# Kernel tuning notes

Measured on AMD Instinct MI355X. Metric: run time of the kernel, lower is better.

The kernel has to match this reference:

```python
import itertools
import jax, jax.numpy as jnp
import numpy as np

N_OBJECTS = 32
GRAPHLET_SIZE = 3
N_FILTERS = 16
REL_DIM = 16
BATCH = 32
N_GROUP_QUERIES = 512
BETA = 1.0

# static combinatorial groups: all C(32,3) = 4960 index triples
GROUP_IDX = jnp.asarray(
    np.array(list(itertools.combinations(range(N_OBJECTS), GRAPHLET_SIZE)), dtype=np.int32)
)  # (G, g)


def setup_inputs() -> dict:
    key = jax.random.key(0)
    k1, k2, k3 = jax.random.split(key, 3)
    inputs = jax.random.normal(k1, (BATCH, N_OBJECTS, N_OBJECTS, REL_DIM), dtype=jnp.float32)
    group_logits = jax.random.normal(k2, (N_GROUP_QUERIES, N_OBJECTS), dtype=jnp.float32)
    filters = jax.random.normal(k3, (N_FILTERS, GRAPHLET_SIZE, GRAPHLET_SIZE, REL_DIM), dtype=jnp.float32)
    return {"inputs": inputs, "group_logits": group_logits, "filters": filters}


def reference(inputs, group_logits, filters):
    idx = GROUP_IDX  # (G, g)
    # gather sub-relation tensors for every group in one fused advanced-index:
    # (B, G, g, g, D)
    sub_rel = inputs[:, idx[:, :, None], idx[:, None, :], :]
    # relational inner product with all filters: (B, G, F)
    rel_conv = jnp.einsum('bgijd,fijd->bgf', sub_rel, filters)
    # soft group weights
    sp = jax.nn.softplus(group_logits)            # (Gi, N)
    group_obj_w = sp[:, idx]                      # (Gi, G, g) -- gather along object axis
    group_w = jnp.prod(group_obj_w, axis=-1)      # (Gi, G)
    norm_w = jax.nn.softmax(BETA * group_w, axis=-1)  # (Gi, G)
    # contract over combinatorial groups: (B, Gi, F)
    out = jnp.einsum('bnr,gn->bgr', rel_conv, norm_w)
    return out
```

## Files before the change

### kernel.cpp

```cpp
#include <hip/hip_runtime.h>
#include <hip/hip_bf16.h>

#define N_OBJ   32
#define G_TOTAL 4960
#define GPAD    5120
#define N_FILT  16
#define REL_D   16
#define BATCH   32
#define NQ      512
#define ZSPLIT  16
#define KCH     320
#define NIT     10

typedef __attribute__((ext_vector_type(8))) short bf16x8;
typedef __attribute__((ext_vector_type(4))) float f32x4;

static __device__ inline unsigned short f2bf(float x) {
    union { float f; unsigned int u; } v; v.f = x;
    unsigned int r = v.u + 0x7fffu + ((v.u >> 16) & 1u);
    return (unsigned short)(r >> 16);
}
static __device__ inline float bfbits2f(unsigned int bits) {
    union { unsigned int u; float f; } v; v.u = bits; return v.f;
}
static __device__ inline void gload_lds16(const void* g, void* l) {
    __builtin_amdgcn_global_load_lds(
        (const __attribute__((address_space(1))) unsigned int*)g,
        (__attribute__((address_space(3))) unsigned int*)(unsigned int)(uintptr_t)l,
        16, 0, 0);
}
static __device__ inline void unrank3(int g, int& a, int& b, int& c) {
    int rem = g;
    for (a = 0; a < 30; a++) { int cnt = ((31 - a) * (30 - a)) >> 1; if (rem < cnt) break; rem -= cnt; }
    for (b = a + 1; b < 31; b++) { if (rem < 31 - b) break; rem -= 31 - b; }
    c = b + 1 + rem;
}

__global__ __launch_bounds__(256) void k_front(const float* __restrict__ logits,
                                               const float* __restrict__ inputs,
                                               const float* __restrict__ filters,
                                               unsigned short* __restrict__ normw,
                                               unsigned short* __restrict__ D) {
    __shared__ __align__(16) char smem[11648];
    int t = threadIdx.x;
    int role = blockIdx.x;

    if (role < NQ) {
        float* sp  = (float*)smem;
        float* red = (float*)(smem + 128);
        unsigned short* wrow = (unsigned short*)(smem + 144);
        int q = role;
        if (t < N_OBJ) {
            float x = logits[q * N_OBJ + t];
            sp[t] = (x > 15.f) ? x : log1pf(expf(x));
        }
        if (t < GPAD - G_TOTAL) wrow[G_TOTAL + t] = 0;
        __syncthreads();

        int g0 = t * 20;
        int aa, bb, cc;
        unrank3(g0, aa, bb, cc);

        float w[20];
        float lmax = -1e30f;
#pragma unroll
        for (int k = 0; k < 20; k++) {
            float v = -1e30f;
            if (g0 + k < G_TOTAL) v = sp[aa] * sp[bb] * sp[cc];
            w[k] = v;
            lmax = fmaxf(lmax, v);
            cc++;
            if (cc >= 32) { bb++; cc = bb + 1; if (cc >= 32) { aa++; bb = aa + 1; cc = bb + 1; } }
        }
#pragma unroll
        for (int off = 32; off; off >>= 1) lmax = fmaxf(lmax, __shfl_down(lmax, off, 64));
        if ((t & 63) == 0) red[t >> 6] = lmax;
        __syncthreads();
        float wmax = fmaxf(fmaxf(red[0], red[1]), fmaxf(red[2], red[3]));

        float lsum = 0.f;
#pragma unroll
        for (int k = 0; k < 20; k++) {
            float e = (g0 + k < G_TOTAL) ? expf(w[k] - wmax) : 0.f;
            w[k] = e;
            lsum += e;
        }
#pragma unroll
        for (int off = 32; off; off >>= 1) lsum += __shfl_down(lsum, off, 64);
        __syncthreads();
        if ((t & 63) == 0) red[t >> 6] = lsum;
        __syncthreads();
        float inv = 1.f / (red[0] + red[1] + red[2] + red[3]);

#pragma unroll
        for (int k = 0; k < 20; k++)
            if (g0 + k < G_TOTAL) wrow[g0 + k] = f2bf(w[k] * inv);
        __syncthreads();
        uint4* dstrow = (uint4*)(normw + (size_t)q * GPAD);
        const uint4* srow = (const uint4*)wrow;
        for (int i = t; i < 640; i += 256) dstrow[i] = srow[i];
    } else {
        float* flt = (float*)smem;
        int bid = role - NQ;
        int p = bid >> 7;
        int xb = bid & 127;
        for (int i = t; i < 576; i += 256) {
            int i4 = i * 4;
            int f = i4 / 144;
            int r = i4 - f * 144;
            *(float4*)&flt[f * 180 + (r >> 4) * 20 + (r & 15)] = *(const float4*)(filters + i4);
        }
        __syncthreads();

        int row = xb * 256 + t;
        int b = row >> 10, xy = row & 1023;
        const float4* src = (const float4*)(inputs + (size_t)row * 16);
        float4 s0 = src[0], s1 = src[1], s2 = src[2], s3 = src[3];

        unsigned short outv[16];
        const float* fb = &flt[p * 20];
#pragma unroll
        for (int f = 0; f < 16; f++) {
            float4 f0 = *(const float4*)(fb + f * 180);
            float4 f1 = *(const float4*)(fb + f * 180 + 4);
            float4 f2 = *(const float4*)(fb + f * 180 + 8);
            float4 f3 = *(const float4*)(fb + f * 180 + 12);
            float d = s0.x * f0.x + s0.y * f0.y + s0.z * f0.z + s0.w * f0.w;
            d += s1.x * f1.x + s1.y * f1.y + s1.z * f1.z + s1.w * f1.w;
            d += s2.x * f2.x + s2.y * f2.y + s2.z * f2.z + s2.w * f2.w;
            d += s3.x * f3.x + s3.y * f3.y + s3.z * f3.z + s3.w * f3.w;
            outv[f] = f2bf(d);
        }
        uint4* dst = (uint4*)(D + ((size_t)(xy * 9 + p)) * 512 + b * 16);
        dst[0] = ((uint4*)outv)[0];
        dst[1] = ((uint4*)outv)[1];
    }
}

__global__ __launch_bounds__(256) void k_mid(const unsigned short* __restrict__ D,
                                             unsigned short* __restrict__ relT) {
    __shared__ int tri[8];
    int t = threadIdx.x;
    int g0 = blockIdx.x * 8;
    if (t < 8) {
        int a, b, c;
        unrank3(g0 + t, a, b, c);
        tri[t] = a | (b << 8) | (c << 16);
    }
    __syncthreads();

    float s0[8], s1[8];
#pragma unroll
    for (int g = 0; g < 8; g++) {
        int pk = tri[g];
        int xs[3] = { pk & 255, (pk >> 8) & 255, (pk >> 16) & 255 };
        float x0 = 0.f, x1 = 0.f;
#pragma unroll
        for (int i = 0; i < 3; i++)
#pragma unroll
            for (int j = 0; j < 3; j++) {
                int xy = xs[i] * 32 + xs[j];
                unsigned int v = *(const unsigned int*)(D + (size_t)(xy * 9 + i * 3 + j) * 512 + t * 2);
                x0 += bfbits2f(v << 16);
                x1 += bfbits2f(v & 0xffff0000u);
            }
        s0[g] = x0; s1[g] = x1;
    }
    unsigned int pack0[4], pack1[4];
#pragma unroll
    for (int k = 0; k < 4; k++) {
        pack0[k] = f2bf(s0[2 * k]) | ((unsigned int)f2bf(s0[2 * k + 1]) << 16);
        pack1[k] = f2bf(s1[2 * k]) | ((unsigned int)f2bf(s1[2 * k + 1]) << 16);
    }
    *(uint4*)(relT + (size_t)(2 * t) * GPAD + g0)     = *(uint4*)pack0;
    *(uint4*)(relT + (size_t)(2 * t + 1) * GPAD + g0) = *(uint4*)pack1;
}

__global__ __launch_bounds__(256) void k_gemm(const unsigned short* __restrict__ A,
                                              const unsigned short* __restrict__ Bm,
                                              float* __restrict__ part) {
    __shared__ __align__(16) unsigned short As[2][64 * 32];
    __shared__ __align__(16) unsigned short Bs[2][64 * 32];
    int tid = threadIdx.x;
    int q0 = blockIdx.x * 64, n0 = blockIdx.y * 64, z = blockIdx.z;
    int k0 = z * KCH;
    int wave = tid >> 6, lane = tid & 63;
    int wm = wave & 1, wn = wave >> 1;
    int row16 = lane & 15, quad = lane >> 4;

    int srow = tid >> 2;
    int schunk = (tid & 3) ^ ((srow >> 1) & 3);
    const unsigned short* ga = A + (size_t)(q0 + srow) * GPAD + k0 + schunk * 8;
    const unsigned short* gb = Bm + (size_t)(n0 + srow) * GPAD + k0 + schunk * 8;
    char* lA = (char*)&As[0][0] + tid * 16;
    char* lB = (char*)&Bs[0][0] + tid * 16;

    f32x4 acc[2][2] = {};
    int fchunk = (quad ^ ((row16 >> 1) & 3)) * 8;

    gload_lds16(ga, lA);
    gload_lds16(gb, lB);
    for (int it = 0; it < NIT; ++it) {
        __syncthreads();
        if (it + 1 < NIT) {
            int nb = (it + 1) & 1;
            gload_lds16(ga + (it + 1) * 32, lA + nb * 64 * 32 * 2);
            gload_lds16(gb + (it + 1) * 32, lB + nb * 64 * 32 * 2);
        }
        int buf = it & 1;
        bf16x8 afr[2], bfr[2];
#pragma unroll
        for (int mi = 0; mi < 2; mi++)
            afr[mi] = *(const bf16x8*)&As[buf][(wm * 32 + mi * 16 + row16) * 32 + fchunk];
#pragma unroll
        for (int ni = 0; ni < 2; ni++)
            bfr[ni] = *(const bf16x8*)&Bs[buf][(wn * 32 + ni * 16 + row16) * 32 + fchunk];
#pragma unroll
        for (int mi = 0; mi < 2; mi++)
#pragma unroll
            for (int ni = 0; ni < 2; ni++)
                acc[mi][ni] = __builtin_amdgcn_mfma_f32_16x16x32_bf16(
                    afr[mi], bfr[ni], acc[mi][ni], 0, 0, 0);
    }

    float* pz = part + (size_t)z * (NQ * 512);
#pragma unroll
    for (int mi = 0; mi < 2; mi++)
#pragma unroll
        for (int ni = 0; ni < 2; ni++)
#pragma unroll
            for (int r = 0; r < 4; r++) {
                int q = q0 + wm * 32 + mi * 16 + quad * 4 + r;
                int n = n0 + wn * 32 + ni * 16 + row16;
                pz[q * 512 + n] = acc[mi][ni][r];
            }
}

__global__ __launch_bounds__(256) void k_reduce(const float* __restrict__ part,
                                                float* __restrict__ out) {
    int gid = blockIdx.x * 256 + threadIdx.x;
    int q = gid >> 7;
    int n = (gid & 127) * 4;
    float4 a = *(const float4*)(part + q * 512 + n);
#pragma unroll
    for (int zz = 1; zz < ZSPLIT; zz++) {
        float4 b4 = *(const float4*)(part + (size_t)zz * (NQ * 512) + q * 512 + n);
        a.x += b4.x; a.y += b4.y; a.z += b4.z; a.w += b4.w;
    }
    *(float4*)(out + (size_t)(n >> 4) * (NQ * REL_D) + q * 16 + (n & 15)) = a;
}

extern "C" void kernel_launch(void* const* d_in, const int* in_sizes, int n_in,
                              void* d_out, int out_size, void* d_ws, size_t ws_size,
                              hipStream_t stream) {
    const float* inputs  = (const float*)d_in[0];
    const float* logits  = (const float*)d_in[1];
    const float* filters = (const float*)d_in[2];
    float* out = (float*)d_out;

    char* ws = (char*)d_ws;
    unsigned short* normw = (unsigned short*)ws;
    unsigned short* D     = (unsigned short*)(ws + 5242880);
    unsigned short* relT  = (unsigned short*)(ws + 14680064);
    float*          part  = (float*)(ws + 19922944);

    k_front<<<NQ + 1152, 256, 0, stream>>>(logits, inputs, filters, normw, D);
    k_mid<<<G_TOTAL / 8, 256, 0, stream>>>(D, relT);
    k_gemm<<<dim3(8, 8, ZSPLIT), 256, 0, stream>>>(normw, relT, part);
    k_reduce<<<NQ * 512 / 4 / 256, 256, 0, stream>>>(part, out);
}
```

Measured before the change: 94.87 us.

## Fuse group gather into GEMM and replace split-K reduce with atomics

Merges the group-gather kernel, the split-K GEMM and the reduction kernel into one back kernel. Each block builds its bf16 relation tile for 160 groups straight into LDS and runs MFMA against normalized weights read from global memory. Partial results go to the output through float atomicAdd, and extra front-kernel blocks zero the output first. This removes the relT and partial-buffer round trips and two launches, at the cost of only 248 blocks at occupancy 1, unstaged A-operand global loads, and heavy atomic traffic.

```diff
diff --git a/kernel.cpp b/kernel.cpp
--- a/kernel.cpp
+++ b/kernel.cpp
@@ -8,9 +8,9 @@
 #define REL_D   16
 #define BATCH   32
 #define NQ      512
-#define ZSPLIT  16
-#define KCH     320
-#define NIT     10
+#define ZBLK    31
+#define KCH     160
+#define BPAD    184
 
 typedef __attribute__((ext_vector_type(8))) short bf16x8;
 typedef __attribute__((ext_vector_type(4))) float f32x4;
@@ -22,12 +22,6 @@
 }
 static __device__ inline float bfbits2f(unsigned int bits) {
     union { unsigned int u; float f; } v; v.u = bits; return v.f;
-}
-static __device__ inline void gload_lds16(const void* g, void* l) {
-    __builtin_amdgcn_global_load_lds(
-        (const __attribute__((address_space(1))) unsigned int*)g,
-        (__attribute__((address_space(3))) unsigned int*)(unsigned int)(uintptr_t)l,
-        16, 0, 0);
 }
 static __device__ inline void unrank3(int g, int& a, int& b, int& c) {
     int rem = g;
@@ -40,7 +34,8 @@
                                                const float* __restrict__ inputs,
                                                const float* __restrict__ filters,
                                                unsigned short* __restrict__ normw,
-                                               unsigned short* __restrict__ D) {
+                                               unsigned short* __restrict__ D,
+                                               float* __restrict__ out) {
     __shared__ __align__(16) char smem[11648];
     int t = threadIdx.x;
     int role = blockIdx.x;
@@ -99,7 +94,7 @@
         uint4* dstrow = (uint4*)(normw + (size_t)q * GPAD);
         const uint4* srow = (const uint4*)wrow;
         for (int i = t; i < 640; i += 256) dstrow[i] = srow[i];
-    } else {
+    } else if (role < NQ + 1152) {
         float* flt = (float*)smem;
         int bid = role - NQ;
         int p = bid >> 7;
@@ -113,12 +108,12 @@
         __syncthreads();
 
         int row = xb * 256 + t;
-        int b = row >> 10, xy = row & 1023;
         const float4* src = (const float4*)(inputs + (size_t)row * 16);
         float4 s0 = src[0], s1 = src[1], s2 = src[2], s3 = src[3];
 
         unsigned short outv[16];
         const float* fb = &flt[p * 20];
+        int xy = row & 1023, b = row >> 10;
 #pragma unroll
         for (int f = 0; f < 16; f++) {
             float4 f0 = *(const float4*)(fb + f * 180);
@@ -134,120 +129,94 @@
         uint4* dst = (uint4*)(D + ((size_t)(xy * 9 + p)) * 512 + b * 16);
         dst[0] = ((uint4*)outv)[0];
         dst[1] = ((uint4*)outv)[1];
-    }
-}
-
-__global__ __launch_bounds__(256) void k_mid(const unsigned short* __restrict__ D,
-                                             unsigned short* __restrict__ relT) {
-    __shared__ int tri[8];
+    } else {
+        int zb = role - (NQ + 1152);
+        uint4 zz; zz.x = zz.y = zz.z = zz.w = 0u;
+        uint4* dst = (uint4*)out + (size_t)zb * 4096;
+#pragma unroll
+        for (int k = 0; k < 16; k++) dst[k * 256 + t] = zz;
+    }
+}
+
+__global__ __launch_bounds__(256, 1) void k_back(const unsigned short* __restrict__ A,
+                                                 const unsigned short* __restrict__ D,
+                                                 float* __restrict__ out) {
+    __shared__ int tri[KCH];
+    __shared__ __align__(16) unsigned short Bs[64][BPAD];
     int t = threadIdx.x;
-    int g0 = blockIdx.x * 8;
-    if (t < 8) {
-        int a, b, c;
-        unrank3(g0 + t, a, b, c);
+    int n0 = blockIdx.x;
+    int z  = blockIdx.y;
+    int g0 = z * KCH;
+
+    if (t < KCH) {
+        int a, b, c; unrank3(g0 + t, a, b, c);
         tri[t] = a | (b << 8) | (c << 16);
     }
     __syncthreads();
 
-    float s0[8], s1[8];
-#pragma unroll
-    for (int g = 0; g < 8; g++) {
-        int pk = tri[g];
-        int xs[3] = { pk & 255, (pk >> 8) & 255, (pk >> 16) & 255 };
-        float x0 = 0.f, x1 = 0.f;
-#pragma unroll
-        for (int i = 0; i < 3; i++)
-#pragma unroll
-            for (int j = 0; j < 3; j++) {
-                int xy = xs[i] * 32 + xs[j];
-                unsigned int v = *(const unsigned int*)(D + (size_t)(xy * 9 + i * 3 + j) * 512 + t * 2);
-                x0 += bfbits2f(v << 16);
-                x1 += bfbits2f(v & 0xffff0000u);
-            }
-        s0[g] = x0; s1[g] = x1;
-    }
-    unsigned int pack0[4], pack1[4];
-#pragma unroll
-    for (int k = 0; k < 4; k++) {
-        pack0[k] = f2bf(s0[2 * k]) | ((unsigned int)f2bf(s0[2 * k + 1]) << 16);
-        pack1[k] = f2bf(s1[2 * k]) | ((unsigned int)f2bf(s1[2 * k + 1]) << 16);
-    }
-    *(uint4*)(relT + (size_t)(2 * t) * GPAD + g0)     = *(uint4*)pack0;
-    *(uint4*)(relT + (size_t)(2 * t + 1) * GPAD + g0) = *(uint4*)pack1;
-}
-
-__global__ __launch_bounds__(256) void k_gemm(const unsigned short* __restrict__ A,
-                                              const unsigned short* __restrict__ Bm,
-                                              float* __restrict__ part) {
-    __shared__ __align__(16) unsigned short As[2][64 * 32];
-    __shared__ __align__(16) unsigned short Bs[2][64 * 32];
-    int tid = threadIdx.x;
-    int q0 = blockIdx.x * 64, n0 = blockIdx.y * 64, z = blockIdx.z;
-    int k0 = z * KCH;
-    int wave = tid >> 6, lane = tid & 63;
-    int wm = wave & 1, wn = wave >> 1;
+    int nsub = t & 31;
+    int gslot = t >> 5;
+    const unsigned short* dbase = D + n0 * 64 + 2 * nsub;
+#pragma unroll 1
+    for (int gp = 0; gp < 10; gp++) {
+        int gl = gslot * 20 + gp * 2;
+        float x0[2], x1[2];
+#pragma unroll
+        for (int gg = 0; gg < 2; gg++) {
+            int pk = tri[gl + gg];
+            int xs[3] = { pk & 255, (pk >> 8) & 255, (pk >> 16) & 255 };
+            float a0 = 0.f, a1 = 0.f;
+#pragma unroll
+            for (int i = 0; i < 3; i++)
+#pragma unroll
+                for (int j = 0; j < 3; j++) {
+                    unsigned int v = *(const unsigned int*)(dbase +
+                        (size_t)((xs[i] * 32 + xs[j]) * 9 + i * 3 + j) * 512);
+                    a0 += bfbits2f(v << 16);
+                    a1 += bfbits2f(v & 0xffff0000u);
+                }
+            x0[gg] = a0; x1[gg] = a1;
+        }
+        unsigned int p0 = f2bf(x0[0]) | ((unsigned int)f2bf(x0[1]) << 16);
+        unsigned int p1 = f2bf(x1[0]) | ((unsigned int)f2bf(x1[1]) << 16);
+        *(unsigned int*)&Bs[2 * nsub][gl]     = p0;
+        *(unsigned int*)&Bs[2 * nsub + 1][gl] = p1;
+    }
+    __syncthreads();
+
+    int wave = t >> 6, lane = t & 63;
+    int qh = wave & 1, nh = wave >> 1;
     int row16 = lane & 15, quad = lane >> 4;
 
-    int srow = tid >> 2;
-    int schunk = (tid & 3) ^ ((srow >> 1) & 3);
-    const unsigned short* ga = A + (size_t)(q0 + srow) * GPAD + k0 + schunk * 8;
-    const unsigned short* gb = Bm + (size_t)(n0 + srow) * GPAD + k0 + schunk * 8;
-    char* lA = (char*)&As[0][0] + tid * 16;
-    char* lB = (char*)&Bs[0][0] + tid * 16;
-
-    f32x4 acc[2][2] = {};
-    int fchunk = (quad ^ ((row16 >> 1) & 3)) * 8;
-
-    gload_lds16(ga, lA);
-    gload_lds16(gb, lB);
-    for (int it = 0; it < NIT; ++it) {
-        __syncthreads();
-        if (it + 1 < NIT) {
-            int nb = (it + 1) & 1;
-            gload_lds16(ga + (it + 1) * 32, lA + nb * 64 * 32 * 2);
-            gload_lds16(gb + (it + 1) * 32, lB + nb * 64 * 32 * 2);
-        }
-        int buf = it & 1;
-        bf16x8 afr[2], bfr[2];
-#pragma unroll
-        for (int mi = 0; mi < 2; mi++)
-            afr[mi] = *(const bf16x8*)&As[buf][(wm * 32 + mi * 16 + row16) * 32 + fchunk];
-#pragma unroll
-        for (int ni = 0; ni < 2; ni++)
-            bfr[ni] = *(const bf16x8*)&Bs[buf][(wn * 32 + ni * 16 + row16) * 32 + fchunk];
-#pragma unroll
-        for (int mi = 0; mi < 2; mi++)
-#pragma unroll
-            for (int ni = 0; ni < 2; ni++)
-                acc[mi][ni] = __builtin_amdgcn_mfma_f32_16x16x32_bf16(
-                    afr[mi], bfr[ni], acc[mi][ni], 0, 0, 0);
-    }
-
-    float* pz = part + (size_t)z * (NQ * 512);
-#pragma unroll
-    for (int mi = 0; mi < 2; mi++)
-#pragma unroll
-        for (int ni = 0; ni < 2; ni++)
-#pragma unroll
-            for (int r = 0; r < 4; r++) {
-                int q = q0 + wm * 32 + mi * 16 + quad * 4 + r;
-                int n = n0 + wn * 32 + ni * 16 + row16;
-                pz[q * 512 + n] = acc[mi][ni][r];
-            }
-}
-
-__global__ __launch_bounds__(256) void k_reduce(const float* __restrict__ part,
-                                                float* __restrict__ out) {
-    int gid = blockIdx.x * 256 + threadIdx.x;
-    int q = gid >> 7;
-    int n = (gid & 127) * 4;
-    float4 a = *(const float4*)(part + q * 512 + n);
-#pragma unroll
-    for (int zz = 1; zz < ZSPLIT; zz++) {
-        float4 b4 = *(const float4*)(part + (size_t)zz * (NQ * 512) + q * 512 + n);
-        a.x += b4.x; a.y += b4.y; a.z += b4.z; a.w += b4.w;
-    }
-    *(float4*)(out + (size_t)(n >> 4) * (NQ * REL_D) + q * 16 + (n & 15)) = a;
+    f32x4 acc[16][2] = {};
+    const unsigned short* arow = A + (size_t)(qh * 256 + row16) * GPAD + g0 + quad * 8;
+    const unsigned short* b0p = &Bs[nh * 32 + row16][quad * 8];
+    const unsigned short* b1p = &Bs[nh * 32 + 16 + row16][quad * 8];
+
+#pragma unroll 1
+    for (int it = 0; it < 5; it++) {
+        bf16x8 bfr0 = *(const bf16x8*)(b0p + it * 32);
+        bf16x8 bfr1 = *(const bf16x8*)(b1p + it * 32);
+#pragma unroll
+        for (int qf = 0; qf < 16; qf++) {
+            bf16x8 afr = *(const bf16x8*)(arow + (size_t)qf * (16 * GPAD) + it * 32);
+            acc[qf][0] = __builtin_amdgcn_mfma_f32_16x16x32_bf16(afr, bfr0, acc[qf][0], 0, 0, 0);
+            acc[qf][1] = __builtin_amdgcn_mfma_f32_16x16x32_bf16(afr, bfr1, acc[qf][1], 0, 0, 0);
+        }
+    }
+
+    int bbase = n0 * 4 + nh * 2;
+#pragma unroll
+    for (int qf = 0; qf < 16; qf++) {
+        int qb = qh * 256 + qf * 16 + quad * 4;
+#pragma unroll
+        for (int nf = 0; nf < 2; nf++) {
+            float* o = out + (size_t)(bbase + nf) * (NQ * REL_D) + row16;
+#pragma unroll
+            for (int r = 0; r < 4; r++)
+                atomicAdd(o + (qb + r) * REL_D, acc[qf][nf][r]);
+        }
+    }
 }
 
 extern "C" void kernel_launch(void* const* d_in, const int* in_sizes, int n_in,
@@ -261,11 +230,7 @@
     char* ws = (char*)d_ws;
     unsigned short* normw = (unsigned short*)ws;
     unsigned short* D     = (unsigned short*)(ws + 5242880);
-    unsigned short* relT  = (unsigned short*)(ws + 14680064);
-    float*          part  = (float*)(ws + 19922944);
-
-    k_front<<<NQ + 1152, 256, 0, stream>>>(logits, inputs, filters, normw, D);
-    k_mid<<<G_TOTAL / 8, 256, 0, stream>>>(D, relT);
-    k_gemm<<<dim3(8, 8, ZSPLIT), 256, 0, stream>>>(normw, relT, part);
-    k_reduce<<<NQ * 512 / 4 / 256, 256, 0, stream>>>(part, out);
-}
+
+    k_front<<<NQ + 1152 + 16, 256, 0, stream>>>(logits, inputs, filters, normw, D, out);
+    k_back<<<dim3(8, ZBLK), 256, 0, stream>>>(normw, D, out);
+}
```

After: 134.8 us. 1.42x slower.

## Fold group gather into GEMM by projecting softmax weights onto pair slots

Applied to the files above, without the earlier changes.

Drops the k_mid gather kernel. Each query's softmax weights over the 4960 triples are scattered with shared-memory atomics into 9 pair-position weight matrices of 32x32 (K=9216), and the per-pair filter projections are stored transposed so a single GEMM contracts over pair positions. This removes one launch and the relT intermediate with its scattered gather reads. In exchange the GEMM K dimension nearly doubles, k_front writes strided 2-byte transposed stores, and the shared-memory atomics add contention.

```diff
diff --git a/kernel.cpp b/kernel.cpp
--- a/kernel.cpp
+++ b/kernel.cpp
@@ -3,14 +3,14 @@
 
 #define N_OBJ   32
 #define G_TOTAL 4960
-#define GPAD    5120
+#define KTOT    9216
 #define N_FILT  16
 #define REL_D   16
 #define BATCH   32
 #define NQ      512
 #define ZSPLIT  16
-#define KCH     320
-#define NIT     10
+#define KCH     576
+#define NIT     18
 
 typedef __attribute__((ext_vector_type(8))) short bf16x8;
 typedef __attribute__((ext_vector_type(4))) float f32x4;
@@ -19,9 +19,6 @@
     union { float f; unsigned int u; } v; v.f = x;
     unsigned int r = v.u + 0x7fffu + ((v.u >> 16) & 1u);
     return (unsigned short)(r >> 16);
-}
-static __device__ inline float bfbits2f(unsigned int bits) {
-    union { unsigned int u; float f; } v; v.u = bits; return v.f;
 }
 static __device__ inline void gload_lds16(const void* g, void* l) {
     __builtin_amdgcn_global_load_lds(
@@ -39,22 +36,22 @@
 __global__ __launch_bounds__(256) void k_front(const float* __restrict__ logits,
                                                const float* __restrict__ inputs,
                                                const float* __restrict__ filters,
-                                               unsigned short* __restrict__ normw,
-                                               unsigned short* __restrict__ D) {
-    __shared__ __align__(16) char smem[11648];
+                                               unsigned short* __restrict__ W2,
+                                               unsigned short* __restrict__ Dt) {
+    __shared__ __align__(16) char smem[37056];
     int t = threadIdx.x;
     int role = blockIdx.x;
 
     if (role < NQ) {
         float* sp  = (float*)smem;
         float* red = (float*)(smem + 128);
-        unsigned short* wrow = (unsigned short*)(smem + 144);
+        float* W2f = (float*)(smem + 144);
         int q = role;
         if (t < N_OBJ) {
             float x = logits[q * N_OBJ + t];
             sp[t] = (x > 15.f) ? x : log1pf(expf(x));
         }
-        if (t < GPAD - G_TOTAL) wrow[G_TOTAL + t] = 0;
+        for (int i = t; i < KTOT; i += 256) W2f[i] = 0.f;
         __syncthreads();
 
         int g0 = t * 20;
@@ -92,13 +89,57 @@
         __syncthreads();
         float inv = 1.f / (red[0] + red[1] + red[2] + red[3]);
 
-#pragma unroll
-        for (int k = 0; k < 20; k++)
-            if (g0 + k < G_TOTAL) wrow[g0 + k] = f2bf(w[k] * inv);
-        __syncthreads();
-        uint4* dstrow = (uint4*)(normw + (size_t)q * GPAD);
-        const uint4* srow = (const uint4*)wrow;
-        for (int i = t; i < 640; i += 256) dstrow[i] = srow[i];
+        unrank3(g0, aa, bb, cc);
+        float run01 = 0.f;
+        int curab = aa * 32 + bb;
+#pragma unroll
+        for (int k = 0; k < 20; k++) {
+            if (g0 + k < G_TOTAL) {
+                float nwk = w[k] * inv;
+                run01 += nwk;
+                atomicAdd(&W2f[2 * 1024 + aa * 32 + cc], nwk);
+                atomicAdd(&W2f[5 * 1024 + bb * 32 + cc], nwk);
+            }
+            cc++;
+            if (cc >= 32) {
+                if (run01 != 0.f) atomicAdd(&W2f[1 * 1024 + curab], run01);
+                run01 = 0.f;
+                bb++; cc = bb + 1;
+                if (cc >= 32) { aa++; bb = aa + 1; cc = bb + 1; }
+                curab = aa * 32 + bb;
+            }
+        }
+        if (run01 != 0.f) atomicAdd(&W2f[1 * 1024 + curab], run01);
+        __syncthreads();
+
+        for (int i = t; i < 1024; i += 256) {
+            int x = i >> 5, y = i & 31;
+            W2f[3 * 1024 + i] = W2f[1 * 1024 + y * 32 + x];
+            W2f[6 * 1024 + i] = W2f[2 * 1024 + y * 32 + x];
+            W2f[7 * 1024 + i] = W2f[5 * 1024 + y * 32 + x];
+        }
+        if (t < 96) {
+            int which = t >> 5, idx = t & 31;
+            float s = 0.f;
+            if (which == 0) {
+                for (int u = 0; u < 32; u++) s += W2f[1 * 1024 + idx * 32 + u];
+                W2f[idx * 33] = s;
+            } else if (which == 1) {
+                for (int u = 0; u < 32; u++) s += W2f[1 * 1024 + u * 32 + idx];
+                W2f[4 * 1024 + idx * 33] = s;
+            } else {
+                for (int u = 0; u < 32; u++) s += W2f[2 * 1024 + u * 32 + idx];
+                W2f[8 * 1024 + idx * 33] = s;
+            }
+        }
+        __syncthreads();
+
+        unsigned int* dstrow = (unsigned int*)(W2 + (size_t)q * KTOT);
+        for (int i = t; i < KTOT / 2; i += 256) {
+            unsigned int pk = (unsigned int)f2bf(W2f[2 * i]) |
+                              ((unsigned int)f2bf(W2f[2 * i + 1]) << 16);
+            dstrow[i] = pk;
+        }
     } else {
         float* flt = (float*)smem;
         int bid = role - NQ;
@@ -113,12 +154,12 @@
         __syncthreads();
 
         int row = xb * 256 + t;
-        int b = row >> 10, xy = row & 1023;
         const float4* src = (const float4*)(inputs + (size_t)row * 16);
         float4 s0 = src[0], s1 = src[1], s2 = src[2], s3 = src[3];
 
         unsigned short outv[16];
         const float* fb = &flt[p * 20];
+        int xy = row & 1023, b = row >> 10;
 #pragma unroll
         for (int f = 0; f < 16; f++) {
             float4 f0 = *(const float4*)(fb + f * 180);
@@ -131,49 +172,11 @@
             d += s3.x * f3.x + s3.y * f3.y + s3.z * f3.z + s3.w * f3.w;
             outv[f] = f2bf(d);
         }
-        uint4* dst = (uint4*)(D + ((size_t)(xy * 9 + p)) * 512 + b * 16);
-        dst[0] = ((uint4*)outv)[0];
-        dst[1] = ((uint4*)outv)[1];
+        unsigned short* drow = Dt + (p * 1024 + xy);
+#pragma unroll
+        for (int f = 0; f < 16; f++)
+            drow[(size_t)(b * 16 + f) * KTOT] = outv[f];
     }
-}
-
-__global__ __launch_bounds__(256) void k_mid(const unsigned short* __restrict__ D,
-                                             unsigned short* __restrict__ relT) {
-    __shared__ int tri[8];
-    int t = threadIdx.x;
-    int g0 = blockIdx.x * 8;
-    if (t < 8) {
-        int a, b, c;
-        unrank3(g0 + t, a, b, c);
-        tri[t] = a | (b << 8) | (c << 16);
-    }
-    __syncthreads();
-
-    float s0[8], s1[8];
-#pragma unroll
-    for (int g = 0; g < 8; g++) {
-        int pk = tri[g];
-        int xs[3] = { pk & 255, (pk >> 8) & 255, (pk >> 16) & 255 };
-        float x0 = 0.f, x1 = 0.f;
-#pragma unroll
-        for (int i = 0; i < 3; i++)
-#pragma unroll
-            for (int j = 0; j < 3; j++) {
-                int xy = xs[i] * 32 + xs[j];
-                unsigned int v = *(const unsigned int*)(D + (size_t)(xy * 9 + i * 3 + j) * 512 + t * 2);
-                x0 += bfbits2f(v << 16);
-                x1 += bfbits2f(v & 0xffff0000u);
-            }
-        s0[g] = x0; s1[g] = x1;
-    }
-    unsigned int pack0[4], pack1[4];
-#pragma unroll
-    for (int k = 0; k < 4; k++) {
-        pack0[k] = f2bf(s0[2 * k]) | ((unsigned int)f2bf(s0[2 * k + 1]) << 16);
-        pack1[k] = f2bf(s1[2 * k]) | ((unsigned int)f2bf(s1[2 * k + 1]) << 16);
-    }
-    *(uint4*)(relT + (size_t)(2 * t) * GPAD + g0)     = *(uint4*)pack0;
-    *(uint4*)(relT + (size_t)(2 * t + 1) * GPAD + g0) = *(uint4*)pack1;
 }
 
 __global__ __launch_bounds__(256) void k_gemm(const unsigned short* __restrict__ A,
@@ -190,8 +193,8 @@
 
     int srow = tid >> 2;
     int schunk = (tid & 3) ^ ((srow >> 1) & 3);
-    const unsigned short* ga = A + (size_t)(q0 + srow) * GPAD + k0 + schunk * 8;
-    const unsigned short* gb = Bm + (size_t)(n0 + srow) * GPAD + k0 + schunk * 8;
+    const unsigned short* ga = A + (size_t)(q0 + srow) * KTOT + k0 + schunk * 8;
+    const unsigned short* gb = Bm + (size_t)(n0 + srow) * KTOT + k0 + schunk * 8;
     char* lA = (char*)&As[0][0] + tid * 16;
     char* lB = (char*)&Bs[0][0] + tid * 16;
 
@@ -259,13 +262,11 @@
     float* out = (float*)d_out;
 
     char* ws = (char*)d_ws;
-    unsigned short* normw = (unsigned short*)ws;
-    unsigned short* D     = (unsigned short*)(ws + 5242880);
-    unsigned short* relT  = (unsigned short*)(ws + 14680064);
-    float*          part  = (float*)(ws + 19922944);
-
-    k_front<<<NQ + 1152, 256, 0, stream>>>(logits, inputs, filters, normw, D);
-    k_mid<<<G_TOTAL / 8, 256, 0, stream>>>(D, relT);
-    k_gemm<<<dim3(8, 8, ZSPLIT), 256, 0, stream>>>(normw, relT, part);
+    unsigned short* W2 = (unsigned short*)ws;
+    unsigned short* Dt = (unsigned short*)(ws + 9437184);
+    float*          part = (float*)(ws + 18874368);
+
+    k_front<<<NQ + 1152, 256, 0, stream>>>(logits, inputs, filters, W2, Dt);
+    k_gemm<<<dim3(8, 8, ZSPLIT), 256, 0, stream>>>(W2, Dt, part);
     k_reduce<<<NQ * 512 / 4 / 256, 256, 0, stream>>>(part, out);
 }
```

Result: slower. 120.1 us (+26.6%).
